# Kernel tuning notes

Hardware: AMD Instinct MI355X
Metric: run time of the kernel (lower is better)

## Reference

```python
import jax, jax.numpy as jnp
import numpy as np

V, E, H = 32000, 32, 128
B, T = 2, 512


def setup_inputs() -> dict:
    key = jax.random.key(0)
    ks = jax.random.split(key, 12)
    s = lambda k, shape, scale=0.05: jax.random.normal(k, shape, dtype=jnp.float32) * scale
    return {
        "x": jax.random.randint(ks[0], (B, T), 0, V, dtype=jnp.int64),
        "hidden": jnp.zeros((1, B, H), dtype=jnp.float32),
        "embed_table": s(ks[1], (V, E)),
        "W_ih": s(ks[2], (H, E)),
        "W_hh": s(ks[3], (H, H)),
        "b_ih": jnp.zeros((H,), jnp.float32),
        "b_hh": jnp.zeros((H,), jnp.float32),
        "W1": s(ks[4], (H, H)),
        "W2": s(ks[5], (H, H)),
        "v": s(ks[6], (H,)),
        "Wp": s(ks[7], (H, 2 * H)),
        "bp": jnp.zeros((H,), jnp.float32),
        "Wfc": s(ks[8], (V, H)),
        "bfc": jnp.zeros((V,), jnp.float32),
    }


def reference(x, hidden, embed_table, W_ih, W_hh, b_ih, b_hh, W1, W2, v, Wp, bp, Wfc, bfc):
    # Embedding: (B, T, E)
    emb = embed_table[x]

    # Single-layer tanh RNN (batch_first). Precompute input projections.
    xp = jnp.einsum('bte,he->bth', emb, W_ih) + b_ih + b_hh  # (B,T,H)

    def step(h, x_t):  # h: (B,H), x_t: (B,H)
        h_new = jnp.tanh(x_t + h @ W_hh.T)
        return h_new, h_new

    h0 = hidden[0]  # (B,H)
    h_last, rnn_out = jax.lax.scan(step, h0, jnp.swapaxes(xp, 0, 1))
    rnn_out = jnp.swapaxes(rnn_out, 0, 1)  # (B,T,H)
    hidden_out = h_last[None]  # (1,B,H)

    # Additive (Bahdanau) self-attention with causal mask.
    query = rnn_out @ W1.T  # (B,T,H)
    keys = rnn_out @ W2.T   # (B,T,H)
    # scores: (B,T,T) via (B,T,T,H) broadcast as in the original module
    scores = jnp.einsum('btsh,h->bts', jnp.tanh(query[:, :, None, :] + keys[:, None, :, :]), v)
    causal = jnp.triu(jnp.ones((T, T), bool), k=1)  # mask future s > t
    scores = jnp.where(causal[None], -jnp.inf, scores)
    weights = jax.nn.softmax(scores, axis=-1)
    weights = jnp.nan_to_num(weights)
    context = jnp.einsum('bts,bsh->bth', weights, rnn_out)

    combined = jnp.concatenate([rnn_out, context], axis=-1)  # (B,T,2H)
    out = jax.nn.relu(combined @ Wp.T + bp)  # dropout is identity in eval
    logits = out @ Wfc.T + bfc  # (B,T,V)
    return logits, hidden_out, weights
```

## Files before the change

kernel.cpp:

```cpp
#include <hip/hip_runtime.h>
#include <hip/hip_bf16.h>

#define T 512
#define H 128
#define V 32000
#define B 2
#define CH 64

typedef __attribute__((ext_vector_type(8))) short bf16x8;
typedef __attribute__((ext_vector_type(4))) float f32x4;

__device__ __forceinline__ unsigned short f2bf(float f){
  unsigned int u = __float_as_uint(f);
  u = (u + 0x7FFFu + ((u >> 16) & 1u)) >> 16;
  return (unsigned short)u;
}

__device__ __forceinline__ float fast_tanh(float x){
  float e = __expf(2.f * x);
  return 1.f - __fdividef(2.f, e + 1.f);
}

__device__ __forceinline__ float quad_reduce_add(float x){
  int y1 = __builtin_amdgcn_mov_dpp(__float_as_int(x), 0xB1, 0xF, 0xF, true);
  float s1 = x + __int_as_float(y1);
  int y2 = __builtin_amdgcn_mov_dpp(__float_as_int(s1), 0x4E, 0xF, 0xF, true);
  return s1 + __int_as_float(y2);
}

__device__ __forceinline__ int hswz(int k){
  return ((k >> 2) & 7) * 16 + ((k >> 5) << 2) + (k & 3);
}

__device__ __forceinline__ void gload_lds16(const float* g, float* l){
  __builtin_amdgcn_global_load_lds((const __attribute__((address_space(1))) void*)g,
                                   (__attribute__((address_space(3))) void*)l, 16, 0, 0);
}

__global__ __launch_bounds__(128) void prep_kernel(const int* __restrict__ x,
    const float* __restrict__ table, const float* __restrict__ W_ih,
    const float* __restrict__ b_ih, const float* __restrict__ b_hh,
    const float* __restrict__ Wfc,
    float* __restrict__ xp, unsigned short* __restrict__ wfcb){
  int blk = blockIdx.x;
  int tid = threadIdx.x;
  __shared__ __align__(16) float e[32];
  if (blk < B * T){
    if (tid < 32) e[tid] = table[(size_t)x[blk] * 32 + tid];
    __syncthreads();
    const float* wr = W_ih + tid * 32;
    float a0 = 0.f, a1 = 0.f, a2 = 0.f, a3 = 0.f;
    #pragma unroll
    for (int k = 0; k < 32; k += 4){
      float4 w4 = *(const float4*)(wr + k);
      float4 e4 = *(const float4*)(e + k);
      a0 += w4.x * e4.x; a1 += w4.y * e4.y; a2 += w4.z * e4.z; a3 += w4.w * e4.w;
    }
    xp[(size_t)blk * H + tid] = (a0 + a1) + (a2 + a3) + b_ih[tid] + b_hh[tid];
  } else {
    size_t base = (size_t)(blk - B * T) * 1024 + (size_t)tid * 8;
    float4 f0 = *(const float4*)(Wfc + base);
    float4 f1 = *(const float4*)(Wfc + base + 4);
    ushort4 o0, o1;
    o0.x = f2bf(f0.x); o0.y = f2bf(f0.y); o0.z = f2bf(f0.z); o0.w = f2bf(f0.w);
    o1.x = f2bf(f1.x); o1.y = f2bf(f1.y); o1.z = f2bf(f1.z); o1.w = f2bf(f1.w);
    *(ushort4*)(wfcb + base) = o0;
    *(ushort4*)(wfcb + base + 4) = o1;
  }
}

__global__ __launch_bounds__(256, 1) void rnn_kernel(const float* __restrict__ xp,
    const float* __restrict__ hidden, const float* __restrict__ W_hh,
    float* __restrict__ rnn, float* __restrict__ hid_out){
  int b = blockIdx.x;
  int tid = threadIdx.x;
  int qp = tid >> 2, q = tid & 3;
  int wv = tid >> 6;
  int r0 = 2 * qp;
  const float* wra = W_hh + (size_t)r0 * H + q * 32;
  const float* wrb = wra + H;
  f32x4 A0 = *(const f32x4*)(wra);
  f32x4 A1 = *(const f32x4*)(wra + 4);
  f32x4 A2 = *(const f32x4*)(wra + 8);
  f32x4 A3 = *(const f32x4*)(wra + 12);
  f32x4 A4 = *(const f32x4*)(wra + 16);
  f32x4 A5 = *(const f32x4*)(wra + 20);
  f32x4 A6 = *(const f32x4*)(wra + 24);
  f32x4 A7 = *(const f32x4*)(wra + 28);
  f32x4 B0 = *(const f32x4*)(wrb);
  f32x4 B1 = *(const f32x4*)(wrb + 4);
  f32x4 B2 = *(const f32x4*)(wrb + 8);
  f32x4 B3 = *(const f32x4*)(wrb + 12);
  f32x4 B4 = *(const f32x4*)(wrb + 16);
  f32x4 B5 = *(const f32x4*)(wrb + 20);
  f32x4 B6 = *(const f32x4*)(wrb + 24);
  f32x4 B7 = *(const f32x4*)(wrb + 28);
  asm volatile("" : "+v"(A0), "+v"(A1), "+v"(A2), "+v"(A3),
                    "+v"(A4), "+v"(A5), "+v"(A6), "+v"(A7));
  asm volatile("" : "+v"(B0), "+v"(B1), "+v"(B2), "+v"(B3),
                    "+v"(B4), "+v"(B5), "+v"(B6), "+v"(B7));

  __shared__ __align__(16) float xs[2][CH][H];
  __shared__ __align__(16) float hist[CH][H];
  __shared__ __align__(16) float hb[2][H];

  const float* xpb = xp + (size_t)b * T * H;

  #pragma unroll
  for (int is = 0; is < 8; ++is)
    gload_lds16(xpb + is * 1024 + tid * 4, &xs[0][0][0] + is * 1024 + wv * 256);
  if (tid < H) hb[0][hswz(tid)] = hidden[b * H + tid];
  __syncthreads();

  int wpos = hswz(r0);
  float hn0 = 0.f, hn1 = 0.f;
  int cur = 0, buf = 0;
  for (int chunk = 0; chunk < T / CH; ++chunk){
    if (chunk + 1 < T / CH){
      const float* src = xpb + (size_t)(chunk + 1) * CH * H;
      #pragma unroll
      for (int is = 0; is < 8; ++is)
        gload_lds16(src + is * 1024 + tid * 4, &xs[buf ^ 1][0][0] + is * 1024 + wv * 256);
    }
    for (int s = 0; s < CH; ++s){
      float2 xv = *(const float2*)(&xs[buf][s][r0]);
      const float* hs = &hb[cur][q * 4];
      float a0 = 0.f, a1 = 0.f, b0 = 0.f, b1 = 0.f;
#define FMA8(n) { f32x4 hv = *(const f32x4*)(hs + 16 * n); \
    a0 = fmaf(hv.x, A##n.x, a0); a1 = fmaf(hv.y, A##n.y, a1); \
    a0 = fmaf(hv.z, A##n.z, a0); a1 = fmaf(hv.w, A##n.w, a1); \
    b0 = fmaf(hv.x, B##n.x, b0); b1 = fmaf(hv.y, B##n.y, b1); \
    b0 = fmaf(hv.z, B##n.z, b0); b1 = fmaf(hv.w, B##n.w, b1); }
      FMA8(0) FMA8(1) FMA8(2) FMA8(3) FMA8(4) FMA8(5) FMA8(6) FMA8(7)
#undef FMA8
      float sa = quad_reduce_add(a0 + a1);
      float sb = quad_reduce_add(b0 + b1);
      hn0 = fast_tanh(xv.x + sa);
      hn1 = fast_tanh(xv.y + sb);
      if (q == 0){
        float2 hw; hw.x = hn0; hw.y = hn1;
        *(float2*)(&hb[cur ^ 1][wpos]) = hw;
      }
      if (q == 1){
        float2 hw; hw.x = hn0; hw.y = hn1;
        *(float2*)(&hist[s][r0]) = hw;
      }
      __syncthreads();
      cur ^= 1;
    }
    {
      const float* hsrc = &hist[0][0];
      float* dst = rnn + (size_t)b * T * H + (size_t)chunk * CH * H;
      #pragma unroll
      for (int r = 0; r < 8; ++r)
        *(float4*)(dst + r * 1024 + tid * 4) = *(const float4*)(hsrc + r * 1024 + tid * 4);
    }
    buf ^= 1;
    __syncthreads();
  }
  if (q == 0){
    float2 hw; hw.x = hn0; hw.y = hn1;
    *(float2*)(&hid_out[b * H + r0]) = hw;
  }
}

__global__ __launch_bounds__(256) void qk_kernel(const float* __restrict__ rnn,
    const float* __restrict__ W1, const float* __restrict__ W2,
    float* __restrict__ q, float* __restrict__ ky){
  int bt = blockIdx.x;
  int tid = threadIdx.x;
  __shared__ __align__(16) float r[H];
  if (tid < H) r[tid] = rnn[(size_t)bt * H + tid];
  __syncthreads();
  int i = tid & (H - 1);
  const float* wrow = ((tid < H) ? W1 : W2) + (size_t)i * H;
  float a0 = 0.f, a1 = 0.f, a2 = 0.f, a3 = 0.f;
  #pragma unroll 8
  for (int k = 0; k < H; k += 4){
    float4 w4 = *(const float4*)(wrow + k);
    float4 r4 = *(const float4*)(r + k);
    a0 += w4.x * r4.x; a1 += w4.y * r4.y; a2 += w4.z * r4.z; a3 += w4.w * r4.w;
  }
  float res = (a0 + a1) + (a2 + a3);
  if (tid < H) q[(size_t)bt * H + i] = res;
  else         ky[(size_t)bt * H + i] = res;
}

__global__ __launch_bounds__(256) void attn_kernel(const float* __restrict__ rnn,
    const float* __restrict__ q, const float* __restrict__ ky,
    const float* __restrict__ v, const float* __restrict__ Wp,
    const float* __restrict__ bp, float* __restrict__ wout,
    unsigned short* __restrict__ outb){
  int bt = blockIdx.x;
  int b = bt >> 9, t = bt & (T - 1);
  int tid = threadIdx.x;
  __shared__ __align__(16) float qL[H], vL[H], rrL[H], ctxL[H];
  __shared__ __align__(16) float ctx2[2][H];
  __shared__ __align__(16) float scL[T], wL[T];
  __shared__ float red[4], red2[4];
  if (tid < H){
    qL[tid]  = q[(size_t)bt * H + tid];
    vL[tid]  = v[tid];
    rrL[tid] = rnn[(size_t)bt * H + tid];
  }
  __syncthreads();
  for (int s = tid; s < T; s += 256){
    float sc = -1e30f;
    if (s <= t){
      const float* kr = ky + (size_t)(b * T + s) * H;
      float a0 = 0.f, a1 = 0.f, a2 = 0.f, a3 = 0.f;
      #pragma unroll 4
      for (int h = 0; h < H; h += 4){
        float4 kv = *(const float4*)(kr + h);
        float4 qv = *(const float4*)(qL + h);
        float4 vv = *(const float4*)(vL + h);
        a0 += fast_tanh(qv.x + kv.x) * vv.x;
        a1 += fast_tanh(qv.y + kv.y) * vv.y;
        a2 += fast_tanh(qv.z + kv.z) * vv.z;
        a3 += fast_tanh(qv.w + kv.w) * vv.w;
      }
      sc = (a0 + a1) + (a2 + a3);
    }
    scL[s] = sc;
  }
  __syncthreads();
  float m = -1e30f;
  for (int s = tid; s < T; s += 256) m = fmaxf(m, scL[s]);
  #pragma unroll
  for (int o = 32; o > 0; o >>= 1) m = fmaxf(m, __shfl_xor(m, o));
  if ((tid & 63) == 0) red[tid >> 6] = m;
  __syncthreads();
  float mx = fmaxf(fmaxf(red[0], red[1]), fmaxf(red[2], red[3]));
  float ls = 0.f;
  for (int s = tid; s < T; s += 256){
    float e = (s <= t) ? __expf(scL[s] - mx) : 0.f;
    wL[s] = e; ls += e;
  }
  #pragma unroll
  for (int o = 32; o > 0; o >>= 1) ls += __shfl_xor(ls, o);
  if ((tid & 63) == 0) red2[tid >> 6] = ls;
  __syncthreads();
  float inv = 1.f / (red2[0] + red2[1] + red2[2] + red2[3]);
  for (int s = tid; s < T; s += 256){
    float wv = wL[s] * inv;
    wL[s] = wv;
    wout[(size_t)bt * T + s] = wv;
  }
  __syncthreads();
  {
    int i2 = tid & (H - 1), hf = tid >> 7;
    const float* rb = rnn + (size_t)b * T * H + i2;
    float c0 = 0.f, c1 = 0.f, c2 = 0.f, c3 = 0.f;
    int s = hf;
    for (; s + 6 <= t; s += 8){
      c0 += wL[s]     * rb[(size_t)s * H];
      c1 += wL[s + 2] * rb[(size_t)(s + 2) * H];
      c2 += wL[s + 4] * rb[(size_t)(s + 4) * H];
      c3 += wL[s + 6] * rb[(size_t)(s + 6) * H];
    }
    for (; s <= t; s += 2) c0 += wL[s] * rb[(size_t)s * H];
    ctx2[hf][i2] = (c0 + c1) + (c2 + c3);
  }
  __syncthreads();
  if (tid < H) ctxL[tid] = ctx2[0][tid] + ctx2[1][tid];
  __syncthreads();
  if (tid < H){
    const float* wp = Wp + (size_t)tid * (2 * H);
    float a0 = 0.f, a1 = 0.f, a2 = 0.f, a3 = 0.f;
    #pragma unroll 8
    for (int k = 0; k < H; k += 4){
      float4 w4 = *(const float4*)(wp + k);
      float4 r4 = *(const float4*)(rrL + k);
      a0 += w4.x * r4.x; a1 += w4.y * r4.y; a2 += w4.z * r4.z; a3 += w4.w * r4.w;
    }
    #pragma unroll 8
    for (int k = 0; k < H; k += 4){
      float4 w4 = *(const float4*)(wp + H + k);
      float4 c4 = *(const float4*)(ctxL + k);
      a0 += w4.x * c4.x; a1 += w4.y * c4.y; a2 += w4.z * c4.z; a3 += w4.w * c4.w;
    }
    float o = bp[tid] + (a0 + a1) + (a2 + a3);
    o = fmaxf(o, 0.f);
    outb[(size_t)bt * H + tid] = f2bf(o);
  }
}

__global__ __launch_bounds__(256, 1) void gemm_kernel(const unsigned short* __restrict__ Ab,
    const unsigned short* __restrict__ Bb, const float* __restrict__ bfc,
    float* __restrict__ Cout){
  int tid = threadIdx.x;
  int l = tid & 63, wv = tid >> 6;
  int lm = l & 15, lq = l >> 4;
  int nBase = blockIdx.x * 128;
  bf16x8 bw[32];
  const unsigned short* bp = Bb + (size_t)(nBase + lm) * H + lq * 8;
  #pragma unroll
  for (int sub = 0; sub < 8; ++sub)
    #pragma unroll
    for (int kk = 0; kk < 4; ++kk)
      bw[sub * 4 + kk] = *(const bf16x8*)(bp + (size_t)sub * 16 * H + kk * 32);
  float bias[8];
  #pragma unroll
  for (int sub = 0; sub < 8; ++sub) bias[sub] = bfc[nBase + lm + sub * 16];
  #pragma unroll 1
  for (int mb = 0; mb < 16; ++mb){
    int rowA = mb * 64 + wv * 16 + lm;
    const unsigned short* ap = Ab + (size_t)rowA * H + lq * 8;
    bf16x8 af[4];
    #pragma unroll
    for (int kk = 0; kk < 4; ++kk) af[kk] = *(const bf16x8*)(ap + kk * 32);
    f32x4 acc[8];
    #pragma unroll
    for (int s = 0; s < 8; ++s) acc[s] = (f32x4){0.f, 0.f, 0.f, 0.f};
    #pragma unroll
    for (int kk = 0; kk < 4; ++kk)
      #pragma unroll
      for (int sub = 0; sub < 8; ++sub)
        acc[sub] = __builtin_amdgcn_mfma_f32_16x16x32_bf16(af[kk], bw[sub * 4 + kk], acc[sub], 0, 0, 0);
    int row0 = mb * 64 + wv * 16 + lq * 4;
    #pragma unroll
    for (int sub = 0; sub < 8; ++sub){
      int c = nBase + lm + sub * 16;
      #pragma unroll
      for (int r = 0; r < 4; ++r)
        Cout[(size_t)(row0 + r) * V + c] = acc[sub][r] + bias[sub];
    }
  }
}

extern "C" void kernel_launch(void* const* d_in, const int* in_sizes, int n_in,
                              void* d_out, int out_size, void* d_ws, size_t ws_size,
                              hipStream_t stream){
  const int*   x      = (const int*)d_in[0];
  const float* hidden = (const float*)d_in[1];
  const float* table  = (const float*)d_in[2];
  const float* W_ih   = (const float*)d_in[3];
  const float* W_hh   = (const float*)d_in[4];
  const float* b_ih   = (const float*)d_in[5];
  const float* b_hh   = (const float*)d_in[6];
  const float* W1     = (const float*)d_in[7];
  const float* W2     = (const float*)d_in[8];
  const float* v      = (const float*)d_in[9];
  const float* Wp     = (const float*)d_in[10];
  const float* bp     = (const float*)d_in[11];
  const float* Wfc    = (const float*)d_in[12];
  const float* bfc    = (const float*)d_in[13];

  float* out     = (float*)d_out;
  float* logits  = out;
  float* hid_out = out + (size_t)B * T * V;
  float* w_out   = hid_out + (size_t)B * H;

  float* xp  = (float*)d_ws;
  float* rnn = xp  + (size_t)B * T * H;
  float* q   = rnn + (size_t)B * T * H;
  float* ky  = q   + (size_t)B * T * H;
  unsigned short* outb = (unsigned short*)(ky + (size_t)B * T * H);
  unsigned short* wfcb = outb + (size_t)B * T * H;

  prep_kernel<<<B * T + (V * H) / 1024, 128, 0, stream>>>(x, table, W_ih, b_ih, b_hh, Wfc, xp, wfcb);
  rnn_kernel<<<B, 256, 0, stream>>>(xp, hidden, W_hh, rnn, hid_out);
  qk_kernel<<<B * T, 256, 0, stream>>>(rnn, W1, W2, q, ky);
  attn_kernel<<<B * T, 256, 0, stream>>>(rnn, q, ky, v, Wp, bp, w_out, outb);
  gemm_kernel<<<V / 128, 256, 0, stream>>>(outb, wfcb, bfc, logits);
}
```

Baseline: 448.5 us.

## Overlap Wfc bf16 conversion with RNN blocks and stage GEMM output via LDS

Moves the Wfc fp32-to-bf16 conversion out of the prep kernel and into extra blocks of the serial RNN kernel. Those blocks can then run on otherwise idle CUs while the two latency-bound recurrence blocks execute. Separately, the logits GEMM now stages each 64x128 output tile in shared memory and writes rows with contiguous float2 stores, replacing the previously scattered per-element stores. The cost is a 33KB LDS buffer per block and the added LDS round trip. There is also some risk that the conversion blocks delay RNN block scheduling.

Measured after the change: 444.8 us. About the same (-0.8%).

```diff
diff --git a/kernel.cpp b/kernel.cpp
--- a/kernel.cpp
+++ b/kernel.cpp
@@ -40,38 +40,38 @@
 __global__ __launch_bounds__(128) void prep_kernel(const int* __restrict__ x,
     const float* __restrict__ table, const float* __restrict__ W_ih,
     const float* __restrict__ b_ih, const float* __restrict__ b_hh,
-    const float* __restrict__ Wfc,
-    float* __restrict__ xp, unsigned short* __restrict__ wfcb){
+    float* __restrict__ xp){
   int blk = blockIdx.x;
   int tid = threadIdx.x;
   __shared__ __align__(16) float e[32];
-  if (blk < B * T){
-    if (tid < 32) e[tid] = table[(size_t)x[blk] * 32 + tid];
-    __syncthreads();
-    const float* wr = W_ih + tid * 32;
-    float a0 = 0.f, a1 = 0.f, a2 = 0.f, a3 = 0.f;
-    #pragma unroll
-    for (int k = 0; k < 32; k += 4){
-      float4 w4 = *(const float4*)(wr + k);
-      float4 e4 = *(const float4*)(e + k);
-      a0 += w4.x * e4.x; a1 += w4.y * e4.y; a2 += w4.z * e4.z; a3 += w4.w * e4.w;
-    }
-    xp[(size_t)blk * H + tid] = (a0 + a1) + (a2 + a3) + b_ih[tid] + b_hh[tid];
-  } else {
-    size_t base = (size_t)(blk - B * T) * 1024 + (size_t)tid * 8;
-    float4 f0 = *(const float4*)(Wfc + base);
-    float4 f1 = *(const float4*)(Wfc + base + 4);
-    ushort4 o0, o1;
-    o0.x = f2bf(f0.x); o0.y = f2bf(f0.y); o0.z = f2bf(f0.z); o0.w = f2bf(f0.w);
-    o1.x = f2bf(f1.x); o1.y = f2bf(f1.y); o1.z = f2bf(f1.z); o1.w = f2bf(f1.w);
-    *(ushort4*)(wfcb + base) = o0;
-    *(ushort4*)(wfcb + base + 4) = o1;
-  }
+  if (tid < 32) e[tid] = table[(size_t)x[blk] * 32 + tid];
+  __syncthreads();
+  const float* wr = W_ih + tid * 32;
+  float a0 = 0.f, a1 = 0.f, a2 = 0.f, a3 = 0.f;
+  #pragma unroll
+  for (int k = 0; k < 32; k += 4){
+    float4 w4 = *(const float4*)(wr + k);
+    float4 e4 = *(const float4*)(e + k);
+    a0 += w4.x * e4.x; a1 += w4.y * e4.y; a2 += w4.z * e4.z; a3 += w4.w * e4.w;
+  }
+  xp[(size_t)blk * H + tid] = (a0 + a1) + (a2 + a3) + b_ih[tid] + b_hh[tid];
 }
 
 __global__ __launch_bounds__(256, 1) void rnn_kernel(const float* __restrict__ xp,
     const float* __restrict__ hidden, const float* __restrict__ W_hh,
-    float* __restrict__ rnn, float* __restrict__ hid_out){
+    const float* __restrict__ Wfc, float* __restrict__ rnn,
+    float* __restrict__ hid_out, unsigned short* __restrict__ wfcb){
+  if (blockIdx.x >= B){
+    size_t base = (size_t)(blockIdx.x - B) * 4096;
+    #pragma unroll
+    for (int j = 0; j < 4; ++j){
+      size_t off = base + (size_t)j * 1024 + (size_t)threadIdx.x * 4;
+      float4 f = *(const float4*)(Wfc + off);
+      ushort4 o; o.x = f2bf(f.x); o.y = f2bf(f.y); o.z = f2bf(f.z); o.w = f2bf(f.w);
+      *(ushort4*)(wfcb + off) = o;
+    }
+    return;
+  }
   int b = blockIdx.x;
   int tid = threadIdx.x;
   int qp = tid >> 2, q = tid & 3;
@@ -292,6 +292,7 @@
   int l = tid & 63, wv = tid >> 6;
   int lm = l & 15, lq = l >> 4;
   int nBase = blockIdx.x * 128;
+  __shared__ __align__(16) float cst[64][132];
   bf16x8 bw[32];
   const unsigned short* bp = Bb + (size_t)(nBase + lm) * H + lq * 8;
   #pragma unroll
@@ -317,13 +318,17 @@
       #pragma unroll
       for (int sub = 0; sub < 8; ++sub)
         acc[sub] = __builtin_amdgcn_mfma_f32_16x16x32_bf16(af[kk], bw[sub * 4 + kk], acc[sub], 0, 0, 0);
-    int row0 = mb * 64 + wv * 16 + lq * 4;
-    #pragma unroll
-    for (int sub = 0; sub < 8; ++sub){
-      int c = nBase + lm + sub * 16;
+    int lrow = wv * 16 + lq * 4;
+    #pragma unroll
+    for (int sub = 0; sub < 8; ++sub)
       #pragma unroll
       for (int r = 0; r < 4; ++r)
-        Cout[(size_t)(row0 + r) * V + c] = acc[sub][r] + bias[sub];
+        cst[lrow + r][lm + sub * 16] = acc[sub][r] + bias[sub];
+    int grow0 = mb * 64 + wv * 16;
+    #pragma unroll
+    for (int rr = 0; rr < 16; ++rr){
+      float2 vv = *(const float2*)(&cst[wv * 16 + rr][l * 2]);
+      *(float2*)(&Cout[(size_t)(grow0 + rr) * V + nBase + l * 2]) = vv;
     }
   }
 }
@@ -358,8 +363,8 @@
   unsigned short* outb = (unsigned short*)(ky + (size_t)B * T * H);
   unsigned short* wfcb = outb + (size_t)B * T * H;
 
-  prep_kernel<<<B * T + (V * H) / 1024, 128, 0, stream>>>(x, table, W_ih, b_ih, b_hh, Wfc, xp, wfcb);
-  rnn_kernel<<<B, 256, 0, stream>>>(xp, hidden, W_hh, rnn, hid_out);
+  prep_kernel<<<B * T, 128, 0, stream>>>(x, table, W_ih, b_ih, b_hh, xp);
+  rnn_kernel<<<B + (V * H) / 4096, 256, 0, stream>>>(xp, hidden, W_hh, Wfc, rnn, hid_out, wfcb);
   qk_kernel<<<B * T, 256, 0, stream>>>(rnn, W1, W2, q, ky);
   attn_kernel<<<B * T, 256, 0, stream>>>(rnn, q, ky, v, Wp, bp, w_out, outb);
   gemm_kernel<<<V / 128, 256, 0, stream>>>(outb, wfcb, bfc, logits);
```
